# Kernel optimization log

Hardware: AMD Instinct MI355X
Metric: run time of the kernel (lower is better)

Reference implementation:

```python
import jax, jax.numpy as jnp
import numpy as np

H = 1024  # hidden_size
NH = 16   # num_heads
HD = H // NH  # head_dim

def setup_inputs() -> dict:
    key = jax.random.key(0)
    ks = jax.random.split(key, 7)
    s = 1.0 / np.sqrt(H)
    return {
        "hidden": jax.random.normal(ks[0], (2, 2048, H), dtype=jnp.float32),
        "Wq": jax.random.normal(ks[1], (H, H), dtype=jnp.float32) * s,
        "bq": jnp.zeros((H,), dtype=jnp.float32),
        "Wk": jax.random.normal(ks[2], (H, H), dtype=jnp.float32) * s,
        "bk": jnp.zeros((H,), dtype=jnp.float32),
        "Wv": jax.random.normal(ks[3], (H, H), dtype=jnp.float32) * s,
        "bv": jnp.zeros((H,), dtype=jnp.float32),
    }

def _split_heads(x):
    # [B, S, H] -> [B, NH, S, HD]
    b, s, _ = x.shape
    return x.reshape(b, s, NH, HD).transpose(0, 2, 1, 3)

def reference(hidden, Wq, bq, Wk, bk, Wv, bv):
    q = _split_heads(hidden @ Wq.T + bq)
    k = _split_heads(hidden @ Wk.T + bk)
    v = _split_heads(hidden @ Wv.T + bv)
    scores = jnp.einsum("bhqd,bhkd->bhqk", q, k) / jnp.sqrt(jnp.float32(HD))
    probs = jax.nn.softmax(scores, axis=-1)  # dropout is identity in eval
    ctx = jnp.einsum("bhqk,bhkd->bhqd", probs, v)
    b, _, s, _ = ctx.shape
    return ctx.transpose(0, 2, 1, 3).reshape(b, s, NH * HD)
```

## Files before the change

### kernel.cpp

```cpp
#include <hip/hip_runtime.h>


typedef __attribute__((ext_vector_type(8))) short bf16x8;
typedef __attribute__((ext_vector_type(4))) short bf16x4;
typedef __attribute__((ext_vector_type(4))) float f32x4;

#define L2E 1.44269504088896340736f

__device__ __forceinline__ f32x4 mfma16(bf16x4 a, bf16x4 b, f32x4 c) {
#if defined(__AMDGCN__)
  return __builtin_amdgcn_mfma_f32_16x16x16bf16_1k(a, b, c, 0, 0, 0);
#else
  return c;
#endif
}

__device__ __forceinline__ unsigned short f2bf(float x) {
  union { float f; unsigned int u; } a; a.f = x;
  unsigned int r = (a.u + 0x7fffu + ((a.u >> 16) & 1u)) >> 16;
  return (unsigned short)r;
}
__device__ __forceinline__ unsigned int fbits(float x) {
  union { float f; unsigned int u; } a; a.f = x; return a.u;
}

__device__ __forceinline__ bf16x4 pack_bf16x4(float p0, float p1, float p2, float p3) {
#if defined(__AMDGCN__) && __has_builtin(__builtin_amdgcn_cvt_pk_bf16_f32)
  typedef __attribute__((ext_vector_type(2))) __bf16 bf16x2_t;
  union { bf16x2_t h[2]; bf16x4 v; } pk;
  pk.h[0] = __builtin_amdgcn_cvt_pk_bf16_f32(p0, p1);
  pk.h[1] = __builtin_amdgcn_cvt_pk_bf16_f32(p2, p3);
  return pk.v;
#else
  unsigned u0 = fbits(p0) + 0x8000u, u1 = fbits(p1) + 0x8000u;
  unsigned u2 = fbits(p2) + 0x8000u, u3 = fbits(p3) + 0x8000u;
  union { unsigned u[2]; bf16x4 v; } pk;
  pk.u[0] = __builtin_amdgcn_perm(u1, u0, 0x07060302u);
  pk.u[1] = __builtin_amdgcn_perm(u3, u2, 0x07060302u);
  return pk.v;
#endif
}

__device__ __forceinline__ void gl_lds16(const unsigned short* g, unsigned short* l) {
  __builtin_amdgcn_global_load_lds(
      (const __attribute__((address_space(1))) void*)g,
      (__attribute__((address_space(3))) void*)l, 16, 0, 0);
}

__global__ __launch_bounds__(256) void convert_all(
    const float* __restrict__ hidden, const float* __restrict__ Wq,
    const float* __restrict__ Wk, const float* __restrict__ Wv,
    unsigned short* __restrict__ Xb, unsigned short* __restrict__ Wqb,
    unsigned short* __restrict__ Wkb, unsigned short* __restrict__ Wvb) {
  int i = blockIdx.x * 256 + threadIdx.x;
  const float* src; unsigned short* dst; int off;
  if (i < 1048576)      { src = hidden; dst = Xb;  off = i; }
  else if (i < 1310720) { src = Wq;     dst = Wqb; off = i - 1048576; }
  else if (i < 1572864) { src = Wk;     dst = Wkb; off = i - 1310720; }
  else                  { src = Wv;     dst = Wvb; off = i - 1572864; }
  float4 v = ((const float4*)src)[off];
  ushort4 o;
  o.x = f2bf(v.x); o.y = f2bf(v.y); o.z = f2bf(v.z); o.w = f2bf(v.w);
  ((ushort4*)dst)[off] = o;
}

__global__ __launch_bounds__(256) void qkv_gemm(
    const unsigned short* __restrict__ Xb,
    const unsigned short* __restrict__ Wqb, const unsigned short* __restrict__ Wkb,
    const unsigned short* __restrict__ Wvb,
    const float* __restrict__ bq, const float* __restrict__ bk,
    const float* __restrict__ bv,
    unsigned short* __restrict__ Qh, unsigned short* __restrict__ Kh,
    unsigned short* __restrict__ Vh) {
  const int id  = blockIdx.x;
  const int xcd = id & 7;
  const int j   = id >> 3;
  const int tok = xcd * 4 + (j & 3);
  const int k2  = j >> 2;
  const int ft  = k2 & 7;
  const int z   = k2 >> 3;

  const unsigned short* Ap; const unsigned short* Bp;
  const float* bias; unsigned short* Out; int m0, n0;
  if (z == 2) {
    Ap = Wvb; Bp = Xb; bias = bv; Out = Vh;
    m0 = ft * 128; n0 = tok * 128;
  } else {
    Ap = Xb; Bp = (z == 0) ? Wqb : Wkb; bias = (z == 0) ? bq : bk;
    Out = (z == 0) ? Qh : Kh;
    m0 = tok * 128; n0 = ft * 128;
  }
  const float oscale = (z == 0) ? (0.125f * L2E) : 1.0f;

  __shared__ unsigned short As[128 * 64];
  __shared__ unsigned short Bs[128 * 64];

  const int tid  = threadIdx.x;
  const int lane = tid & 63;
  const int w    = tid >> 6;
  const int wm   = w >> 1, wn = w & 1;
  const int quad = lane >> 4;
  const int r    = lane & 15;

  f32x4 acc[4][4];
#pragma unroll
  for (int a = 0; a < 4; a++)
#pragma unroll
    for (int c = 0; c < 4; c++) acc[a][c] = (f32x4){0.f, 0.f, 0.f, 0.f};

  for (int k0 = 0; k0 < 1024; k0 += 64) {
    __syncthreads();
#pragma unroll
    for (int i = 0; i < 4; i++) {
      int t   = w * 4 + i;
      int blk = t * 64 + lane;
      int row = blk >> 3;
      int c   = (blk & 7) ^ (row & 7);
      gl_lds16(Ap + (size_t)(m0 + row) * 1024 + k0 + c * 8, &As[t * 512]);
      gl_lds16(Bp + (size_t)(n0 + row) * 1024 + k0 + c * 8, &Bs[t * 512]);
    }
    __syncthreads();

    bf16x8 af[4][2], bfv[4][2];
#pragma unroll
    for (int mi = 0; mi < 4; mi++)
#pragma unroll
      for (int ks = 0; ks < 2; ks++) {
        int row = wm * 64 + mi * 16 + r;
        int bc  = (ks * 4 + quad) ^ (row & 7);
        af[mi][ks] = *(const bf16x8*)&As[row * 64 + bc * 8];
      }
#pragma unroll
    for (int ni = 0; ni < 4; ni++)
#pragma unroll
      for (int ks = 0; ks < 2; ks++) {
        int row = wn * 64 + ni * 16 + r;
        int bc  = (ks * 4 + quad) ^ (row & 7);
        bfv[ni][ks] = *(const bf16x8*)&Bs[row * 64 + bc * 8];
      }
#pragma unroll
    for (int mi = 0; mi < 4; mi++)
#pragma unroll
      for (int ni = 0; ni < 4; ni++) {
        acc[mi][ni] = __builtin_amdgcn_mfma_f32_16x16x32_bf16(af[mi][0], bfv[ni][0], acc[mi][ni], 0, 0, 0);
        acc[mi][ni] = __builtin_amdgcn_mfma_f32_16x16x32_bf16(af[mi][1], bfv[ni][1], acc[mi][ni], 0, 0, 0);
      }
  }

  if (z == 2) {
#pragma unroll
    for (int mi = 0; mi < 4; mi++)
#pragma unroll
      for (int e = 0; e < 4; e++) {
        int m = m0 + wm * 64 + mi * 16 + quad * 4 + e;
        float bm = bias[m];
#pragma unroll
        for (int ni = 0; ni < 4; ni++) {
          int n = n0 + wn * 64 + ni * 16 + r;
          int bb = n >> 11, s = n & 2047;
          int hh = m >> 6,  d = m & 63;
          float v = acc[mi][ni][e] + bm;
          Out[((size_t)(bb * 16 + hh) * 64 + d) * 2048 + s] = f2bf(v);
        }
      }
  } else {
    float biasv[4];
#pragma unroll
    for (int ni = 0; ni < 4; ni++) biasv[ni] = bias[n0 + wn * 64 + ni * 16 + r];
#pragma unroll
    for (int mi = 0; mi < 4; mi++)
#pragma unroll
      for (int ni = 0; ni < 4; ni++)
#pragma unroll
        for (int e = 0; e < 4; e++) {
          int m = m0 + wm * 64 + mi * 16 + quad * 4 + e;
          int n = n0 + wn * 64 + ni * 16 + r;
          int bb = m >> 11, s = m & 2047;
          int hh = n >> 6,  d = n & 63;
          float v = (acc[mi][ni][e] + biasv[ni]) * oscale;
          Out[((size_t)(bb * 16 + hh) * 2048 + s) * 64 + d] = f2bf(v);
        }
  }
}

__global__ __launch_bounds__(512, 8) void attn(
    const unsigned short* __restrict__ Qh, const unsigned short* __restrict__ Kh,
    const unsigned short* __restrict__ Vh, float* __restrict__ Out) {
  const int h = blockIdx.y, b = blockIdx.z;
  const int bh = b * 16 + h;
  const int q0 = blockIdx.x * 64;
  const unsigned short* Qp  = Qh + (size_t)bh * 2048 * 64;
  const unsigned short* Kp  = Kh + (size_t)bh * 2048 * 64;
  const unsigned short* VTp = Vh + (size_t)bh * 64 * 2048;

  __shared__ unsigned short SM[2][2][64 * 64];

  const int tid  = threadIdx.x;
  const int lane = tid & 63;
  const int w8   = tid >> 6;
  const int half = w8 >> 2;
  const int w    = w8 & 3;
  const int ltid = tid & 255;
  const int quad = lane >> 4;
  const int r    = lane & 15;
  const int rm7  = r & 7;

  unsigned short* Ks  = &SM[half][0][0];
  unsigned short* Vts = &SM[half][1][0];

  const unsigned short* qrow = Qp + (size_t)(q0 + w * 16 + r) * 64 + quad * 8;
  bf16x8 aq0 = *(const bf16x8*)(qrow);
  bf16x8 aq1 = *(const bf16x8*)(qrow + 32);

  f32x4 lacc = (f32x4){0.f, 0.f, 0.f, 0.f};
  f32x4 acc[4];
#pragma unroll
  for (int dc = 0; dc < 4; dc++) acc[dc] = (f32x4){0.f, 0.f, 0.f, 0.f};
  const f32x4 zero4 = (f32x4){0.f, 0.f, 0.f, 0.f};

  union { unsigned u[2]; bf16x4 v; } ou;
  ou.u[0] = 0x3F803F80u; ou.u[1] = 0x3F803F80u;
  const bf16x4 ones = ou.v;

  const int kx0 = quad ^ rm7;
  const int kx1 = (4 + quad) ^ rm7;
  const int qh2 = quad >> 1, ql4 = (quad & 1) * 4;

  const int kvbase = half * 1024;
  for (int kv0 = kvbase; kv0 < kvbase + 1024; kv0 += 64) {
    __syncthreads();
#pragma unroll
    for (int i = 0; i < 2; i++) {
      int blk = i * 256 + ltid;
      int row = blk >> 3;
      int cs  = blk & 7;
      gl_lds16(Kp + (size_t)(kv0 + row) * 64 + ((cs ^ (row & 7)) * 8), &Ks[blk * 8]);
      gl_lds16(VTp + (size_t)row * 2048 + kv0 + (((cs + 5 * row) & 7) * 8), &Vts[blk * 8]);
    }
    __syncthreads();

#pragma unroll
    for (int nc = 0; nc < 4; nc++) {
      int krow = nc * 16 + r;
      bf16x8 kf0 = *(const bf16x8*)&Ks[krow * 64 + kx0 * 8];
      bf16x8 kf1 = *(const bf16x8*)&Ks[krow * 64 + kx1 * 8];

      f32x4 t0 = __builtin_amdgcn_mfma_f32_16x16x32_bf16(kf1, aq1, zero4, 0, 0, 0);
      f32x4 sT = __builtin_amdgcn_mfma_f32_16x16x32_bf16(kf0, aq0, t0, 0, 0, 0);

      float p0 = __builtin_exp2f(sT[0]);
      float p1 = __builtin_exp2f(sT[1]);
      float p2 = __builtin_exp2f(sT[2]);
      float p3 = __builtin_exp2f(sT[3]);
      bf16x4 ap = pack_bf16x4(p0, p1, p2, p3);

      lacc = mfma16(ap, ones, lacc);

#pragma unroll
      for (int dc = 0; dc < 4; dc++) {
        int vrow = dc * 16 + r;
        int slot = (2 * nc + qh2 + 3 * vrow) & 7;
        bf16x4 vf = *(const bf16x4*)&Vts[vrow * 64 + slot * 8 + ql4];
        acc[dc] = mfma16(ap, vf, acc[dc]);
      }
    }
  }

  __syncthreads();
  float* Abuf = (float*)&SM[0][0][0];
  float* Lbuf = Abuf + 64 * 65;
  if (half == 1) {
#pragma unroll
    for (int e = 0; e < 4; e++) {
      int q = w * 16 + quad * 4 + e;
#pragma unroll
      for (int dc = 0; dc < 4; dc++)
        Abuf[q * 65 + dc * 16 + r] = acc[dc][e];
      if (r == 0) Lbuf[q] = lacc[e];
    }
  }
  __syncthreads();
  if (half == 0) {
#pragma unroll
    for (int e = 0; e < 4; e++) {
      int q = w * 16 + quad * 4 + e;
      float l = lacc[e] + Lbuf[q];
      float inv = 1.f / l;
      int s = q0 + q;
#pragma unroll
      for (int dc = 0; dc < 4; dc++) {
        int d = dc * 16 + r;
        float v = acc[dc][e] + Abuf[q * 65 + d];
        Out[(size_t)(b * 2048 + s) * 1024 + h * 64 + d] = v * inv;
      }
    }
  }
}

extern "C" void kernel_launch(void* const* d_in, const int* in_sizes, int n_in,
                              void* d_out, int out_size, void* d_ws, size_t ws_size,
                              hipStream_t stream) {
  const float* hidden = (const float*)d_in[0];
  const float* Wq = (const float*)d_in[1];
  const float* bq = (const float*)d_in[2];
  const float* Wk = (const float*)d_in[3];
  const float* bk = (const float*)d_in[4];
  const float* Wv = (const float*)d_in[5];
  const float* bv = (const float*)d_in[6];
  float* out = (float*)d_out;

  char* ws = (char*)d_ws;
  unsigned short* Qhp = (unsigned short*)(ws + 0);
  unsigned short* Khp = (unsigned short*)(ws + 8388608);
  unsigned short* Vhp = (unsigned short*)(ws + 16777216);
  unsigned short* Xb  = (unsigned short*)(ws + 25165824);
  unsigned short* Wqb = (unsigned short*)(ws + 33554432);
  unsigned short* Wkb = (unsigned short*)(ws + 35651584);
  unsigned short* Wvb = (unsigned short*)(ws + 37748736);

  convert_all<<<7168, 256, 0, stream>>>(hidden, Wq, Wk, Wv, Xb, Wqb, Wkb, Wvb);
  qkv_gemm<<<768, 256, 0, stream>>>(Xb, Wqb, Wkb, Wvb, bq, bk, bv,
                                    Qhp, Khp, Vhp);
  attn<<<dim3(32, 16, 2), 512, 0, stream>>>(Qhp, Khp, Vhp, out);
}
```

Before: 184.0 us.

## Load QKV GEMM fragments directly from global memory, dropping LDS staging

```diff
diff --git a/kernel.cpp b/kernel.cpp
--- a/kernel.cpp
+++ b/kernel.cpp
@@ -64,7 +64,7 @@
   ((ushort4*)dst)[off] = o;
 }
 
-__global__ __launch_bounds__(256) void qkv_gemm(
+__global__ __launch_bounds__(256, 3) void qkv_gemm(
     const unsigned short* __restrict__ Xb,
     const unsigned short* __restrict__ Wqb, const unsigned short* __restrict__ Wkb,
     const unsigned short* __restrict__ Wvb,
@@ -92,9 +92,6 @@
   }
   const float oscale = (z == 0) ? (0.125f * L2E) : 1.0f;
 
-  __shared__ unsigned short As[128 * 64];
-  __shared__ unsigned short Bs[128 * 64];
-
   const int tid  = threadIdx.x;
   const int lane = tid & 63;
   const int w    = tid >> 6;
@@ -102,49 +99,29 @@
   const int quad = lane >> 4;
   const int r    = lane & 15;
 
+  const unsigned short* abase = Ap + (size_t)(m0 + wm * 64 + r) * 1024 + quad * 8;
+  const unsigned short* bbase = Bp + (size_t)(n0 + wn * 64 + r) * 1024 + quad * 8;
+
   f32x4 acc[4][4];
 #pragma unroll
   for (int a = 0; a < 4; a++)
 #pragma unroll
     for (int c = 0; c < 4; c++) acc[a][c] = (f32x4){0.f, 0.f, 0.f, 0.f};
 
-  for (int k0 = 0; k0 < 1024; k0 += 64) {
-    __syncthreads();
-#pragma unroll
-    for (int i = 0; i < 4; i++) {
-      int t   = w * 4 + i;
-      int blk = t * 64 + lane;
-      int row = blk >> 3;
-      int c   = (blk & 7) ^ (row & 7);
-      gl_lds16(Ap + (size_t)(m0 + row) * 1024 + k0 + c * 8, &As[t * 512]);
-      gl_lds16(Bp + (size_t)(n0 + row) * 1024 + k0 + c * 8, &Bs[t * 512]);
-    }
-    __syncthreads();
-
-    bf16x8 af[4][2], bfv[4][2];
+#pragma unroll 4
+  for (int k0 = 0; k0 < 1024; k0 += 32) {
+    bf16x8 a[4], bb[4];
 #pragma unroll
     for (int mi = 0; mi < 4; mi++)
-#pragma unroll
-      for (int ks = 0; ks < 2; ks++) {
-        int row = wm * 64 + mi * 16 + r;
-        int bc  = (ks * 4 + quad) ^ (row & 7);
-        af[mi][ks] = *(const bf16x8*)&As[row * 64 + bc * 8];
-      }
+      a[mi] = *(const bf16x8*)(abase + mi * 16384 + k0);
 #pragma unroll
     for (int ni = 0; ni < 4; ni++)
-#pragma unroll
-      for (int ks = 0; ks < 2; ks++) {
-        int row = wn * 64 + ni * 16 + r;
-        int bc  = (ks * 4 + quad) ^ (row & 7);
-        bfv[ni][ks] = *(const bf16x8*)&Bs[row * 64 + bc * 8];
-      }
+      bb[ni] = *(const bf16x8*)(bbase + ni * 16384 + k0);
 #pragma unroll
     for (int mi = 0; mi < 4; mi++)
 #pragma unroll
-      for (int ni = 0; ni < 4; ni++) {
-        acc[mi][ni] = __builtin_amdgcn_mfma_f32_16x16x32_bf16(af[mi][0], bfv[ni][0], acc[mi][ni], 0, 0, 0);
-        acc[mi][ni] = __builtin_amdgcn_mfma_f32_16x16x32_bf16(af[mi][1], bfv[ni][1], acc[mi][ni], 0, 0, 0);
-      }
+      for (int ni = 0; ni < 4; ni++)
+        acc[mi][ni] = __builtin_amdgcn_mfma_f32_16x16x32_bf16(a[mi], bb[ni], acc[mi][ni], 0, 0, 0);
   }
 
   if (z == 2) {
@@ -157,10 +134,10 @@
 #pragma unroll
         for (int ni = 0; ni < 4; ni++) {
           int n = n0 + wn * 64 + ni * 16 + r;
-          int bb = n >> 11, s = n & 2047;
+          int bb2 = n >> 11, s = n & 2047;
           int hh = m >> 6,  d = m & 63;
           float v = acc[mi][ni][e] + bm;
-          Out[((size_t)(bb * 16 + hh) * 64 + d) * 2048 + s] = f2bf(v);
+          Out[((size_t)(bb2 * 16 + hh) * 64 + d) * 2048 + s] = f2bf(v);
         }
       }
   } else {
@@ -175,10 +152,10 @@
         for (int e = 0; e < 4; e++) {
           int m = m0 + wm * 64 + mi * 16 + quad * 4 + e;
           int n = n0 + wn * 64 + ni * 16 + r;
-          int bb = m >> 11, s = m & 2047;
+          int bb2 = m >> 11, s = m & 2047;
           int hh = n >> 6,  d = n & 63;
           float v = (acc[mi][ni][e] + biasv[ni]) * oscale;
-          Out[((size_t)(bb * 16 + hh) * 2048 + s) * 64 + d] = f2bf(v);
+          Out[((size_t)(bb2 * 16 + hh) * 2048 + s) * 64 + d] = f2bf(v);
         }
   }
 }
```

Result: slower. 230.2 us (+25.1%).
